# Kernel optimization log

Hardware: AMD Instinct MI355X
Metric: run time of the kernel (lower is better)

Reference implementation:

```python
import jax, jax.numpy as jnp
import numpy as np

D = 128
EMB = 1024
B, S = 4, 4096


def setup_inputs() -> dict:
    key = jax.random.key(0)
    ks = jax.random.split(key, 7)
    scale = 1.0 / np.sqrt(EMB)
    return {
        "X": jax.random.normal(ks[0], (B, S, EMB), dtype=jnp.float32),
        "lam": jnp.float32(0.8),
        "Wq": jax.random.uniform(ks[1], (EMB, 2 * D), jnp.float32, -scale, scale),
        "bq": jax.random.uniform(ks[2], (2 * D,), jnp.float32, -scale, scale),
        "Wk": jax.random.uniform(ks[3], (EMB, 2 * D), jnp.float32, -scale, scale),
        "bk": jax.random.uniform(ks[4], (2 * D,), jnp.float32, -scale, scale),
        "Wv": jax.random.uniform(ks[5], (EMB, D), jnp.float32, -scale, scale),
        "bv": jax.random.uniform(ks[6], (D,), jnp.float32, -scale, scale),
    }


def reference(X, lam, Wq, bq, Wk, bk, Wv, bv):
    # Projections: Q,K are [B,S,2d]; V is [B,S,d]
    Q = X @ Wq + bq
    K = X @ Wk + bk
    V = X @ Wv + bv
    Q1, Q2 = Q[..., :D], Q[..., D:]
    K1, K2 = K[..., :D], K[..., D:]
    s = 1.0 / jnp.sqrt(jnp.float32(D))
    # Dual QK^T scores [B,S,S]
    A1 = jnp.einsum("bqd,bkd->bqk", Q1, K1) * s
    A2 = jnp.einsum("bqd,bkd->bqk", Q2, K2) * s
    P = jax.nn.softmax(A1, axis=-1) - lam * jax.nn.softmax(A2, axis=-1)
    return jnp.einsum("bqk,bkd->bqd", P, V)
```

## Files before the change

kernel.cpp:

```cpp
#include <hip/hip_runtime.h>
#include <hip/hip_bf16.h>


typedef __attribute__((ext_vector_type(8))) short bf16x8;
typedef __attribute__((ext_vector_type(4))) float f32x4;
typedef __attribute__((ext_vector_type(16))) float f32x16;

#define MFMA16(a, b, c) __builtin_amdgcn_mfma_f32_16x16x32_bf16((a), (b), (c), 0, 0, 0)
#define MFMA32(a, b, c) __builtin_amdgcn_mfma_f32_32x32x16_bf16((a), (b), (c), 0, 0, 0)

typedef const __attribute__((address_space(1))) void gas_void;
typedef __attribute__((address_space(3))) void las_void;
#define GLOAD16(G, L) __builtin_amdgcn_global_load_lds((gas_void*)(G), (las_void*)(L), 16, 0, 0)

__device__ __forceinline__ unsigned short f2bf(float x) {
    union { float f; unsigned u; } v; v.f = x;
    return (unsigned short)((v.u + 0x7FFFu + ((v.u >> 16) & 1u)) >> 16);
}
__device__ __forceinline__ unsigned pk2bf(float a, float b) {
    __hip_bfloat162 h = __float22bfloat162_rn(float2{a, b});
    union { __hip_bfloat162 h2; unsigned u; } cv; cv.h2 = h;
    return cv.u;
}
__device__ __forceinline__ float fexp2(float x) {
    float r; asm("v_exp_f32 %0, %1" : "=v"(r) : "v"(x)); return r;
}

__global__ __launch_bounds__(256) void wtrans_kernel(
    const float* __restrict__ Wq, const float* __restrict__ Wk,
    const float* __restrict__ Wv, unsigned short* __restrict__ Wt) {
    int tid = blockIdx.x * 256 + threadIdx.x;
    int k = tid & 1023, n = tid >> 10;
    float v;
    if (n < 256)      v = Wq[k * 256 + n];
    else if (n < 512) v = Wk[k * 256 + (n - 256)];
    else              v = Wv[k * 128 + (n - 512)];
    Wt[tid] = f2bf(v);
}

__global__ __launch_bounds__(256) void proj_kernel(
    const float* __restrict__ X, const unsigned short* __restrict__ Wt,
    const float* __restrict__ bq, const float* __restrict__ bk,
    const float* __restrict__ bv,
    unsigned short* __restrict__ Qs, unsigned short* __restrict__ Kb,
    unsigned short* __restrict__ Vb) {
    __shared__ alignas(16) char lds[16384];
    const int nt = blockIdx.y;
    const int m0 = blockIdx.x * 128;
    const int t = threadIdx.x, w = t >> 6, l = t & 63, c = l & 15, g = l >> 4;
    const int wm = w >> 1, wn = w & 1;
    const unsigned short* Wrow = Wt + (long)(nt * 128) * 1024;

    f32x4 acc[4][4];
    const f32x4 fz = {0.f, 0.f, 0.f, 0.f};
#pragma unroll
    for (int i = 0; i < 4; i++)
#pragma unroll
        for (int j = 0; j < 4; j++) acc[i][j] = fz;

    const int srow = t >> 1, sh = t & 1;
    const int sswz = (srow & 7) << 4;
    for (int k0 = 0; k0 < 1024; k0 += 32) {
        const float* xs = X + (long)(m0 + srow) * 1024 + k0 + sh * 16;
        float4 f0 = *(const float4*)(xs + 0);
        float4 f1 = *(const float4*)(xs + 4);
        float4 f2 = *(const float4*)(xs + 8);
        float4 f3 = *(const float4*)(xs + 12);
        const unsigned short* wsc = Wrow + (long)srow * 1024 + k0 + sh * 16;
        uint4 w0 = *(const uint4*)(wsc + 0);
        uint4 w1 = *(const uint4*)(wsc + 8);
        uint4 xa, xb;
        xa.x = pk2bf(f0.x, f0.y); xa.y = pk2bf(f0.z, f0.w);
        xa.z = pk2bf(f1.x, f1.y); xa.w = pk2bf(f1.z, f1.w);
        xb.x = pk2bf(f2.x, f2.y); xb.y = pk2bf(f2.z, f2.w);
        xb.z = pk2bf(f3.x, f3.y); xb.w = pk2bf(f3.z, f3.w);
        int base = srow * 64 + sh * 32;
        *(uint4*)(lds + ((base + 0) ^ sswz)) = xa;
        *(uint4*)(lds + ((base + 16) ^ sswz)) = xb;
        *(uint4*)(lds + 8192 + ((base + 0) ^ sswz)) = w0;
        *(uint4*)(lds + 8192 + ((base + 16) ^ sswz)) = w1;
        __syncthreads();

        bf16x8 af[4];
#pragma unroll
        for (int am = 0; am < 4; am++) {
            int r_ = wm * 64 + am * 16 + c;
            af[am] = *(const bf16x8*)(lds + ((r_ * 64 + g * 16) ^ ((c & 7) << 4)));
        }
#pragma unroll
        for (int bn = 0; bn < 4; bn++) {
            int r_ = wn * 64 + bn * 16 + c;
            bf16x8 bfr = *(const bf16x8*)(lds + 8192 + ((r_ * 64 + g * 16) ^ ((c & 7) << 4)));
#pragma unroll
            for (int am = 0; am < 4; am++) acc[am][bn] = MFMA16(af[am], bfr, acc[am][bn]);
        }
        __syncthreads();
    }

    const float QSCALE = 0.08838834764831845f * 1.4426950408889634f;
    const float* bias; float scale; unsigned short* outp; int ostride, ocol0, boff;
    if (nt < 2)      { bias = bq; boff = nt * 128;       scale = QSCALE; outp = Qs; ostride = 256; ocol0 = nt * 128; }
    else if (nt < 4) { bias = bk; boff = (nt - 2) * 128; scale = 1.0f;   outp = Kb; ostride = 256; ocol0 = (nt - 2) * 128; }
    else             { bias = bv; boff = 0;              scale = 1.0f;   outp = Vb; ostride = 128; ocol0 = 0; }
#pragma unroll
    for (int bn = 0; bn < 4; bn++) {
        int ncol = wn * 64 + bn * 16 + c;
        float bb = bias[boff + ncol];
#pragma unroll
        for (int am = 0; am < 4; am++) {
#pragma unroll
            for (int r = 0; r < 4; r++) {
                long row = m0 + wm * 64 + am * 16 + 4 * g + r;
                outp[row * ostride + ocol0 + ncol] = f2bf((acc[am][bn][r] + bb) * scale);
            }
        }
    }
}

__global__ __launch_bounds__(256) void vtrans_kernel(
    const unsigned short* __restrict__ Vb, unsigned short* __restrict__ Vt) {
    int tid = blockIdx.x * 256 + threadIdx.x;
    int s = tid & 4095, d = (tid >> 12) & 127, b = tid >> 19;
    Vt[tid] = Vb[(((long)b << 12) + s) * 128 + d];
}

__global__ __launch_bounds__(256) void attn3_kernel(
    const unsigned short* __restrict__ Qs, const unsigned short* __restrict__ Kb,
    const unsigned short* __restrict__ Vt,
    float* __restrict__ Po, float* __restrict__ Ps, int nsplit, int ks) {
    __shared__ alignas(16) char lds[49152];
    const int t = threadIdx.x;
    const int w = t >> 6, l = t & 63, r31 = l & 31, hi = l >> 5;

    const int total = gridDim.x;
    const int lin = (blockIdx.x & 7) * (total >> 3) + (blockIdx.x >> 3);
    const int qb = lin & 31;
    const int g2 = lin >> 5;
    const int br = g2 & 1;
    const int sp = g2 >> 1;
    const int split = sp % nsplit, b = sp / nsplit;

    const long qrow = (long)b * 4096 + qb * 128 + w * 32 + r31;
    bf16x8 qf[8];
    const unsigned short* Qp = Qs + qrow * 256 + br * 128 + hi * 8;
#pragma unroll
    for (int ds = 0; ds < 8; ds++) qf[ds] = *(const bf16x8*)(Qp + ds * 16);

    f32x16 o[4];
    const f32x16 oz = {};
#pragma unroll
    for (int dt = 0; dt < 4; dt++) o[dt] = oz;
    float m = -1e30f, s = 0.f;

    const int krowA = t >> 4;
    const int kcolS = (((t & 15) * 16) - krowA * 16) & 255;
    const int vdA = t >> 2;
    const int vcolS = (((t & 3) * 16) - (((vdA >> 1) & 3) * 16)) & 63;
    const long kbb = (long)b * 4096;
    const char* kSrc0 = (const char*)Kb + (kbb + krowA) * 512 + br * 256 + kcolS;
    const char* vSrc0 = (const char*)Vt + ((long)b * 128 + vdA) * 8192 + vcolS;
    char* dst0 = lds + w * 1024;

    const int kb0 = split * ks;
    const int nt = ks >> 5;
#define STAGE(KB_, BUF_)                                                       \
    {                                                                          \
        const char* kp_ = kSrc0 + (long)(KB_)*512;                             \
        const char* vp_ = vSrc0 + (long)(KB_)*2;                               \
        char* d_ = dst0 + (BUF_)*16384;                                        \
        GLOAD16(kp_, d_);                                                      \
        GLOAD16(kp_ + 8192, d_ + 4096);                                        \
        GLOAD16(vp_, d_ + 8192);                                               \
        GLOAD16(vp_ + 524288, d_ + 12288);                                     \
    }

    int kro[8];
#pragma unroll
    for (int ds = 0; ds < 8; ds++)
        kro[ds] = r31 * 256 + ((ds * 32 + hi * 16 + r31 * 16) & 255);
    int vro0[4], vro1[4];
#pragma unroll
    for (int dt = 0; dt < 4; dt++) {
        int vr = dt * 32 + r31, rot = ((vr >> 1) & 3) * 16;
        vro0[dt] = 8192 + vr * 64 + ((hi * 16 + rot) & 63);
        vro1[dt] = 8192 + vr * 64 + ((32 + hi * 16 + rot) & 63);
    }

    STAGE(kb0, 0);
    STAGE(kb0 + 32, 1);
    int cb = 0, sb = 2;

    for (int it = 0; it < nt; it++) {
        asm volatile("s_waitcnt vmcnt(4)" ::: "memory");
        __builtin_amdgcn_sched_barrier(0);
        __builtin_amdgcn_s_barrier();
        __builtin_amdgcn_sched_barrier(0);
        {
            int i2 = it + 2;
            int kn = (i2 < nt) ? kb0 + (i2 << 5) : kb0;
            STAGE(kn, sb);
        }
        const char* bufp = lds + cb * 16384;

        f32x16 pa = oz, pb_ = oz;
        __builtin_amdgcn_s_setprio(1);
#pragma unroll
        for (int ds = 0; ds < 4; ds++) {
            bf16x8 kfa = *(const bf16x8*)(bufp + kro[ds]);
            bf16x8 kfb = *(const bf16x8*)(bufp + kro[ds + 4]);
            pa = MFMA32(kfa, qf[ds], pa);
            pb_ = MFMA32(kfb, qf[ds + 4], pb_);
        }
        __builtin_amdgcn_s_setprio(0);
        f32x16 p;
#pragma unroll
        for (int i = 0; i < 16; i++) p[i] = pa[i] + pb_[i];

        float m0_ = fmaxf(fmaxf(p[0], p[1]), p[2]);
        float m1_ = fmaxf(fmaxf(p[3], p[4]), p[5]);
        float m2_ = fmaxf(fmaxf(p[6], p[7]), p[8]);
        float m3_ = fmaxf(fmaxf(p[9], p[10]), p[11]);
        float m4_ = fmaxf(fmaxf(p[12], p[13]), p[14]);
        float lmx = fmaxf(fmaxf(fmaxf(fmaxf(m0_, m1_), m2_),
                                fmaxf(m3_, m4_)), p[15]);
        lmx = fmaxf(lmx, __shfl_xor(lmx, 32));
        if (__any(lmx > m + 8.f)) {
            float mn = fmaxf(m, lmx);
            float al = fexp2(m - mn);
            s *= al; m = mn;
#pragma unroll
            for (int dt = 0; dt < 4; dt++) o[dt] *= al;
        }
        float pe[16];
#pragma unroll
        for (int i = 0; i < 16; i++) pe[i] = fexp2(p[i] - m);
        float s0 = (pe[0] + pe[1]) + (pe[2] + pe[3]);
        float s1 = (pe[4] + pe[5]) + (pe[6] + pe[7]);
        float s2 = (pe[8] + pe[9]) + (pe[10] + pe[11]);
        float s3 = (pe[12] + pe[13]) + (pe[14] + pe[15]);
        float ps_ = (s0 + s1) + (s2 + s3);
        ps_ += __shfl_xor(ps_, 32);
        s += ps_;

        unsigned cA = pk2bf(pe[0], pe[1]), cB = pk2bf(pe[2], pe[3]);
        unsigned cC = pk2bf(pe[4], pe[5]), cD = pk2bf(pe[6], pe[7]);
        asm volatile("v_permlane32_swap_b32 %0, %1" : "+v"(cA), "+v"(cC));
        asm volatile("v_permlane32_swap_b32 %0, %1" : "+v"(cB), "+v"(cD));
        unsigned dA = pk2bf(pe[8], pe[9]), dB = pk2bf(pe[10], pe[11]);
        unsigned dC = pk2bf(pe[12], pe[13]), dD = pk2bf(pe[14], pe[15]);
        asm volatile("v_permlane32_swap_b32 %0, %1" : "+v"(dA), "+v"(dC));
        asm volatile("v_permlane32_swap_b32 %0, %1" : "+v"(dB), "+v"(dD));
        union { uint4 u; bf16x8 v; } pb0, pb1;
        pb0.u = uint4{cA, cB, cC, cD};
        pb1.u = uint4{dA, dB, dC, dD};

        __builtin_amdgcn_s_setprio(1);
#pragma unroll
        for (int dt = 0; dt < 4; dt++) {
            bf16x8 vf0 = *(const bf16x8*)(bufp + vro0[dt]);
            bf16x8 vf1 = *(const bf16x8*)(bufp + vro1[dt]);
            o[dt] = MFMA32(vf0, pb0.v, o[dt]);
            o[dt] = MFMA32(vf1, pb1.v, o[dt]);
        }
        __builtin_amdgcn_s_setprio(0);
        cb = (cb == 2) ? 0 : cb + 1;
        sb = (sb == 2) ? 0 : sb + 1;
    }
    asm volatile("s_waitcnt vmcnt(0)" ::: "memory");

    float* po = Po + ((qrow * nsplit + split) * 2 + br) * 128;
#pragma unroll
    for (int dt = 0; dt < 4; dt++) {
#pragma unroll
        for (int rg = 0; rg < 4; rg++) {
            float4 v;
            v.x = o[dt][rg * 4 + 0];
            v.y = o[dt][rg * 4 + 1];
            v.z = o[dt][rg * 4 + 2];
            v.w = o[dt][rg * 4 + 3];
            *(float4*)(po + dt * 32 + rg * 8 + hi * 4) = v;
        }
    }
    if (hi == 0)
        *(float2*)(Ps + (qrow * nsplit + split) * 4 + br * 2) = float2{m, s};
#undef STAGE
}

__global__ __launch_bounds__(256) void combine_kernel(
    const float* __restrict__ Po, const float* __restrict__ Ps,
    const float* __restrict__ lam_p, float* __restrict__ out, int nsplit) {
    int tid = blockIdx.x * 256 + threadIdx.x;
    int q = tid >> 5, dq = (tid & 31) * 4;
    float M1 = -1e30f, M2 = -1e30f;
    for (int s = 0; s < nsplit; s++) {
        float4 st = *(const float4*)(Ps + (long)(q * nsplit + s) * 4);
        M1 = fmaxf(M1, st.x); M2 = fmaxf(M2, st.z);
    }
    float S1 = 0.f, S2 = 0.f;
    float a0 = 0.f, a1 = 0.f, a2 = 0.f, a3 = 0.f;
    float b0 = 0.f, b1 = 0.f, b2 = 0.f, b3 = 0.f;
    for (int s = 0; s < nsplit; s++) {
        float4 st = *(const float4*)(Ps + (long)(q * nsplit + s) * 4);
        float w1 = fexp2(st.x - M1), w2 = fexp2(st.z - M2);
        S1 += st.y * w1; S2 += st.w * w2;
        const float* p1 = Po + (((long)q * nsplit + s) * 2 + 0) * 128 + dq;
        const float* p2 = Po + (((long)q * nsplit + s) * 2 + 1) * 128 + dq;
        float4 v1 = *(const float4*)p1;
        float4 v2 = *(const float4*)p2;
        a0 += v1.x * w1; a1 += v1.y * w1; a2 += v1.z * w1; a3 += v1.w * w1;
        b0 += v2.x * w2; b1 += v2.y * w2; b2 += v2.z * w2; b3 += v2.w * w2;
    }
    float lam = *lam_p;
    float i1 = 1.f / S1, i2 = lam / S2;
    float4 v;
    v.x = a0 * i1 - b0 * i2;
    v.y = a1 * i1 - b1 * i2;
    v.z = a2 * i1 - b2 * i2;
    v.w = a3 * i1 - b3 * i2;
    *(float4*)(out + (long)q * 128 + dq) = v;
}

extern "C" void kernel_launch(void* const* d_in, const int* in_sizes, int n_in,
                              void* d_out, int out_size, void* d_ws, size_t ws_size,
                              hipStream_t stream) {
    const float* X   = (const float*)d_in[0];
    const float* lam = (const float*)d_in[1];
    const float* Wq  = (const float*)d_in[2];
    const float* bq  = (const float*)d_in[3];
    const float* Wk  = (const float*)d_in[4];
    const float* bk  = (const float*)d_in[5];
    const float* Wv  = (const float*)d_in[6];
    const float* bv  = (const float*)d_in[7];
    char* ws = (char*)d_ws;
    unsigned short* Qs = (unsigned short*)(ws);
    unsigned short* Kb = (unsigned short*)(ws + (8u << 20));
    unsigned short* Vb = (unsigned short*)(ws + (16u << 20));
    unsigned short* Vt = (unsigned short*)(ws + (20u << 20));
    unsigned short* Wt = (unsigned short*)(ws + (24u << 20));
    const size_t base = (size_t)26 << 20;
    const size_t NQ = 16384;
    int nsplit = 1;
    if (ws_size >= base + NQ * 4 * 2 * 128 * 4 + NQ * 4 * 4 * 4)      nsplit = 4;
    else if (ws_size >= base + NQ * 2 * 2 * 128 * 4 + NQ * 2 * 4 * 4) nsplit = 2;
    float* Po = (float*)(ws + base);
    float* Ps = (float*)(ws + base + NQ * (size_t)nsplit * 2 * 128 * 4);

    wtrans_kernel<<<2560, 256, 0, stream>>>(Wq, Wk, Wv, Wt);
    proj_kernel<<<dim3(128, 5), 256, 0, stream>>>(X, Wt, bq, bk, bv, Qs, Kb, Vb);
    vtrans_kernel<<<8192, 256, 0, stream>>>(Vb, Vt);
    attn3_kernel<<<256 * nsplit, 256, 0, stream>>>(Qs, Kb, Vt, Po, Ps,
                                                   nsplit, 4096 / nsplit);
    combine_kernel<<<2048, 256, 0, stream>>>(Po, Ps, lam, (float*)d_out, nsplit);
}
```

Before: 170.8 us.

## Widen attention KV tile to 64 with double buffering; tile V transpose via LDS

The attention loop now processes 64 keys per iteration instead of 32. It uses two 32 KB LDS buffers instead of three 16 KB ones, and sets launch bounds to two blocks per CU. The aim is to halve the barrier count and the softmax bookkeeping per key and to give the MFMA units more independent work. In exchange the prefetch waits for vmcnt(0) at each iteration, so prefetch depth and overlap shrink. Separately, the V transpose becomes a tiled LDS kernel with 16-byte coalesced loads and stores, replacing the scalar strided gather.

```diff
diff --git a/kernel.cpp b/kernel.cpp
--- a/kernel.cpp
+++ b/kernel.cpp
@@ -119,16 +119,35 @@
 
 __global__ __launch_bounds__(256) void vtrans_kernel(
     const unsigned short* __restrict__ Vb, unsigned short* __restrict__ Vt) {
-    int tid = blockIdx.x * 256 + threadIdx.x;
-    int s = tid & 4095, d = (tid >> 12) & 127, b = tid >> 19;
-    Vt[tid] = Vb[(((long)b << 12) + s) * 128 + d];
-}
-
-__global__ __launch_bounds__(256) void attn3_kernel(
+    __shared__ unsigned short lds[64][72];
+    const int bid = blockIdx.x;
+    const int db = bid & 1, sb = (bid >> 1) & 63, b = bid >> 7;
+    const int s0 = sb * 64, d0 = db * 64;
+    const int t = threadIdx.x;
+    const int r = t >> 2, c4 = t & 3;
+    const unsigned short* src = Vb + ((long)(b * 4096 + s0 + r)) * 128 + d0;
+    uint4 u0 = *(const uint4*)(src + c4 * 8);
+    uint4 u1 = *(const uint4*)(src + (c4 + 4) * 8);
+    *(uint4*)(&lds[r][c4 * 8]) = u0;
+    *(uint4*)(&lds[r][(c4 + 4) * 8]) = u1;
+    __syncthreads();
+    const int dd = t >> 2;
+    unsigned short* dst = Vt + ((long)(b * 128 + d0 + dd)) * 4096 + s0;
+#pragma unroll
+    for (int cc2 = 0; cc2 < 2; cc2++) {
+        int cc = c4 + cc2 * 4;
+        unsigned short tmp[8];
+#pragma unroll
+        for (int j = 0; j < 8; j++) tmp[j] = lds[cc * 8 + j][dd];
+        *(uint4*)(dst + cc * 8) = *(const uint4*)tmp;
+    }
+}
+
+__global__ __launch_bounds__(256, 2) void attn3_kernel(
     const unsigned short* __restrict__ Qs, const unsigned short* __restrict__ Kb,
     const unsigned short* __restrict__ Vt,
     float* __restrict__ Po, float* __restrict__ Ps, int nsplit, int ks) {
-    __shared__ alignas(16) char lds[49152];
+    __shared__ alignas(16) char lds[65536];
     const int t = threadIdx.x;
     const int w = t >> 6, l = t & 63, r31 = l & 31, hi = l >> 5;
 
@@ -162,16 +181,20 @@
     char* dst0 = lds + w * 1024;
 
     const int kb0 = split * ks;
-    const int nt = ks >> 5;
+    const int nt = ks >> 6;
 #define STAGE(KB_, BUF_)                                                       \
     {                                                                          \
         const char* kp_ = kSrc0 + (long)(KB_)*512;                             \
         const char* vp_ = vSrc0 + (long)(KB_)*2;                               \
-        char* d_ = dst0 + (BUF_)*16384;                                        \
+        char* d_ = dst0 + (BUF_)*32768;                                        \
         GLOAD16(kp_, d_);                                                      \
         GLOAD16(kp_ + 8192, d_ + 4096);                                        \
-        GLOAD16(vp_, d_ + 8192);                                               \
-        GLOAD16(vp_ + 524288, d_ + 12288);                                     \
+        GLOAD16(kp_ + 16384, d_ + 8192);                                       \
+        GLOAD16(kp_ + 24576, d_ + 12288);                                      \
+        GLOAD16(vp_, d_ + 16384);                                              \
+        GLOAD16(vp_ + 524288, d_ + 20480);                                     \
+        GLOAD16(vp_ + 64, d_ + 24576);                                         \
+        GLOAD16(vp_ + 524288 + 64, d_ + 28672);                                \
     }
 
     int kro[8];
@@ -182,47 +205,48 @@
 #pragma unroll
     for (int dt = 0; dt < 4; dt++) {
         int vr = dt * 32 + r31, rot = ((vr >> 1) & 3) * 16;
-        vro0[dt] = 8192 + vr * 64 + ((hi * 16 + rot) & 63);
-        vro1[dt] = 8192 + vr * 64 + ((32 + hi * 16 + rot) & 63);
+        vro0[dt] = 16384 + vr * 64 + ((hi * 16 + rot) & 63);
+        vro1[dt] = 16384 + vr * 64 + ((32 + hi * 16 + rot) & 63);
     }
 
     STAGE(kb0, 0);
-    STAGE(kb0 + 32, 1);
-    int cb = 0, sb = 2;
 
     for (int it = 0; it < nt; it++) {
-        asm volatile("s_waitcnt vmcnt(4)" ::: "memory");
+        asm volatile("s_waitcnt vmcnt(0)" ::: "memory");
         __builtin_amdgcn_sched_barrier(0);
         __builtin_amdgcn_s_barrier();
         __builtin_amdgcn_sched_barrier(0);
-        {
-            int i2 = it + 2;
-            int kn = (i2 < nt) ? kb0 + (i2 << 5) : kb0;
-            STAGE(kn, sb);
-        }
-        const char* bufp = lds + cb * 16384;
-
-        f32x16 pa = oz, pb_ = oz;
+        if (it + 1 < nt) STAGE(kb0 + ((it + 1) << 6), (it + 1) & 1);
+        const char* bufp = lds + (it & 1) * 32768;
+
+        f32x16 pa0 = oz, pb0_ = oz, pa1 = oz, pb1_ = oz;
         __builtin_amdgcn_s_setprio(1);
 #pragma unroll
         for (int ds = 0; ds < 4; ds++) {
-            bf16x8 kfa = *(const bf16x8*)(bufp + kro[ds]);
-            bf16x8 kfb = *(const bf16x8*)(bufp + kro[ds + 4]);
-            pa = MFMA32(kfa, qf[ds], pa);
-            pb_ = MFMA32(kfb, qf[ds + 4], pb_);
+            bf16x8 k0a = *(const bf16x8*)(bufp + kro[ds]);
+            bf16x8 k0b = *(const bf16x8*)(bufp + kro[ds + 4]);
+            bf16x8 k1a = *(const bf16x8*)(bufp + 8192 + kro[ds]);
+            bf16x8 k1b = *(const bf16x8*)(bufp + 8192 + kro[ds + 4]);
+            pa0 = MFMA32(k0a, qf[ds], pa0);
+            pb0_ = MFMA32(k0b, qf[ds + 4], pb0_);
+            pa1 = MFMA32(k1a, qf[ds], pa1);
+            pb1_ = MFMA32(k1b, qf[ds + 4], pb1_);
         }
         __builtin_amdgcn_s_setprio(0);
-        f32x16 p;
-#pragma unroll
-        for (int i = 0; i < 16; i++) p[i] = pa[i] + pb_[i];
-
-        float m0_ = fmaxf(fmaxf(p[0], p[1]), p[2]);
-        float m1_ = fmaxf(fmaxf(p[3], p[4]), p[5]);
-        float m2_ = fmaxf(fmaxf(p[6], p[7]), p[8]);
-        float m3_ = fmaxf(fmaxf(p[9], p[10]), p[11]);
-        float m4_ = fmaxf(fmaxf(p[12], p[13]), p[14]);
-        float lmx = fmaxf(fmaxf(fmaxf(fmaxf(m0_, m1_), m2_),
-                                fmaxf(m3_, m4_)), p[15]);
+        f32x16 p0, p1;
+#pragma unroll
+        for (int i = 0; i < 16; i++) { p0[i] = pa0[i] + pb0_[i]; p1[i] = pa1[i] + pb1_[i]; }
+
+        float x0 = fmaxf(fmaxf(p0[0], p0[1]), fmaxf(p0[2], p0[3]));
+        float x1 = fmaxf(fmaxf(p0[4], p0[5]), fmaxf(p0[6], p0[7]));
+        float x2 = fmaxf(fmaxf(p0[8], p0[9]), fmaxf(p0[10], p0[11]));
+        float x3 = fmaxf(fmaxf(p0[12], p0[13]), fmaxf(p0[14], p0[15]));
+        float y0 = fmaxf(fmaxf(p1[0], p1[1]), fmaxf(p1[2], p1[3]));
+        float y1 = fmaxf(fmaxf(p1[4], p1[5]), fmaxf(p1[6], p1[7]));
+        float y2 = fmaxf(fmaxf(p1[8], p1[9]), fmaxf(p1[10], p1[11]));
+        float y3 = fmaxf(fmaxf(p1[12], p1[13]), fmaxf(p1[14], p1[15]));
+        float lmx = fmaxf(fmaxf(fmaxf(x0, x1), fmaxf(x2, x3)),
+                          fmaxf(fmaxf(y0, y1), fmaxf(y2, y3)));
         lmx = fmaxf(lmx, __shfl_xor(lmx, 32));
         if (__any(lmx > m + 8.f)) {
             float mn = fmaxf(m, lmx);
@@ -231,42 +255,57 @@
 #pragma unroll
             for (int dt = 0; dt < 4; dt++) o[dt] *= al;
         }
-        float pe[16];
-#pragma unroll
-        for (int i = 0; i < 16; i++) pe[i] = fexp2(p[i] - m);
-        float s0 = (pe[0] + pe[1]) + (pe[2] + pe[3]);
-        float s1 = (pe[4] + pe[5]) + (pe[6] + pe[7]);
-        float s2 = (pe[8] + pe[9]) + (pe[10] + pe[11]);
-        float s3 = (pe[12] + pe[13]) + (pe[14] + pe[15]);
+        float pe0[16], pe1[16];
+#pragma unroll
+        for (int i = 0; i < 16; i++) { pe0[i] = fexp2(p0[i] - m); pe1[i] = fexp2(p1[i] - m); }
+        float s0 = ((pe0[0] + pe0[1]) + (pe0[2] + pe0[3])) +
+                   ((pe0[4] + pe0[5]) + (pe0[6] + pe0[7]));
+        float s1 = ((pe0[8] + pe0[9]) + (pe0[10] + pe0[11])) +
+                   ((pe0[12] + pe0[13]) + (pe0[14] + pe0[15]));
+        float s2 = ((pe1[0] + pe1[1]) + (pe1[2] + pe1[3])) +
+                   ((pe1[4] + pe1[5]) + (pe1[6] + pe1[7]));
+        float s3 = ((pe1[8] + pe1[9]) + (pe1[10] + pe1[11])) +
+                   ((pe1[12] + pe1[13]) + (pe1[14] + pe1[15]));
         float ps_ = (s0 + s1) + (s2 + s3);
         ps_ += __shfl_xor(ps_, 32);
         s += ps_;
 
-        unsigned cA = pk2bf(pe[0], pe[1]), cB = pk2bf(pe[2], pe[3]);
-        unsigned cC = pk2bf(pe[4], pe[5]), cD = pk2bf(pe[6], pe[7]);
+        unsigned cA = pk2bf(pe0[0], pe0[1]), cB = pk2bf(pe0[2], pe0[3]);
+        unsigned cC = pk2bf(pe0[4], pe0[5]), cD = pk2bf(pe0[6], pe0[7]);
         asm volatile("v_permlane32_swap_b32 %0, %1" : "+v"(cA), "+v"(cC));
         asm volatile("v_permlane32_swap_b32 %0, %1" : "+v"(cB), "+v"(cD));
-        unsigned dA = pk2bf(pe[8], pe[9]), dB = pk2bf(pe[10], pe[11]);
-        unsigned dC = pk2bf(pe[12], pe[13]), dD = pk2bf(pe[14], pe[15]);
+        unsigned dA = pk2bf(pe0[8], pe0[9]), dB = pk2bf(pe0[10], pe0[11]);
+        unsigned dC = pk2bf(pe0[12], pe0[13]), dD = pk2bf(pe0[14], pe0[15]);
         asm volatile("v_permlane32_swap_b32 %0, %1" : "+v"(dA), "+v"(dC));
         asm volatile("v_permlane32_swap_b32 %0, %1" : "+v"(dB), "+v"(dD));
-        union { uint4 u; bf16x8 v; } pb0, pb1;
-        pb0.u = uint4{cA, cB, cC, cD};
-        pb1.u = uint4{dA, dB, dC, dD};
+        unsigned eA = pk2bf(pe1[0], pe1[1]), eB = pk2bf(pe1[2], pe1[3]);
+        unsigned eC = pk2bf(pe1[4], pe1[5]), eD = pk2bf(pe1[6], pe1[7]);
+        asm volatile("v_permlane32_swap_b32 %0, %1" : "+v"(eA), "+v"(eC));
+        asm volatile("v_permlane32_swap_b32 %0, %1" : "+v"(eB), "+v"(eD));
+        unsigned fA = pk2bf(pe1[8], pe1[9]), fB = pk2bf(pe1[10], pe1[11]);
+        unsigned fC = pk2bf(pe1[12], pe1[13]), fD = pk2bf(pe1[14], pe1[15]);
+        asm volatile("v_permlane32_swap_b32 %0, %1" : "+v"(fA), "+v"(fC));
+        asm volatile("v_permlane32_swap_b32 %0, %1" : "+v"(fB), "+v"(fD));
+        union { uint4 u; bf16x8 v; } q00, q01, q10, q11;
+        q00.u = uint4{cA, cB, cC, cD};
+        q01.u = uint4{dA, dB, dC, dD};
+        q10.u = uint4{eA, eB, eC, eD};
+        q11.u = uint4{fA, fB, fC, fD};
 
         __builtin_amdgcn_s_setprio(1);
 #pragma unroll
         for (int dt = 0; dt < 4; dt++) {
-            bf16x8 vf0 = *(const bf16x8*)(bufp + vro0[dt]);
-            bf16x8 vf1 = *(const bf16x8*)(bufp + vro1[dt]);
-            o[dt] = MFMA32(vf0, pb0.v, o[dt]);
-            o[dt] = MFMA32(vf1, pb1.v, o[dt]);
+            bf16x8 v00 = *(const bf16x8*)(bufp + vro0[dt]);
+            bf16x8 v01 = *(const bf16x8*)(bufp + vro1[dt]);
+            bf16x8 v10 = *(const bf16x8*)(bufp + 8192 + vro0[dt]);
+            bf16x8 v11 = *(const bf16x8*)(bufp + 8192 + vro1[dt]);
+            o[dt] = MFMA32(v00, q00.v, o[dt]);
+            o[dt] = MFMA32(v01, q01.v, o[dt]);
+            o[dt] = MFMA32(v10, q10.v, o[dt]);
+            o[dt] = MFMA32(v11, q11.v, o[dt]);
         }
         __builtin_amdgcn_s_setprio(0);
-        cb = (cb == 2) ? 0 : cb + 1;
-        sb = (sb == 2) ? 0 : sb + 1;
-    }
-    asm volatile("s_waitcnt vmcnt(0)" ::: "memory");
+    }
 
     float* po = Po + ((qrow * nsplit + split) * 2 + br) * 128;
 #pragma unroll
@@ -347,7 +386,7 @@
 
     wtrans_kernel<<<2560, 256, 0, stream>>>(Wq, Wk, Wv, Wt);
     proj_kernel<<<dim3(128, 5), 256, 0, stream>>>(X, Wt, bq, bk, bv, Qs, Kb, Vb);
-    vtrans_kernel<<<8192, 256, 0, stream>>>(Vb, Vt);
+    vtrans_kernel<<<512, 256, 0, stream>>>(Vb, Vt);
     attn3_kernel<<<256 * nsplit, 256, 0, stream>>>(Qs, Kb, Vt, Po, Ps,
                                                    nsplit, 4096 / nsplit);
     combine_kernel<<<2048, 256, 0, stream>>>(Po, Ps, lam, (float*)d_out, nsplit);
```

Measured after the change: 157.4 us, median of 2. 1.09x faster.

## Split key tiles across wave pairs in attention and tile V transpose through LDS

Applied to the files above, without the earlier changes.

The attention kernel goes from 256 to 512 threads per block. Each pair of waves shares one 32-row query group and handles alternating 32-key tiles, with four LDS buffers loaded two tiles at a time. At the end the partial softmax states of each pair are merged through LDS. The V transpose becomes a tiled LDS transpose with vectorized loads and stores instead of a strided scalar gather. The goal is more waves in flight to hide latency. The costs are larger LDS use, a full vmcnt(0) wait each iteration, and an extra reduction step.

```diff
diff --git a/kernel.cpp b/kernel.cpp
--- a/kernel.cpp
+++ b/kernel.cpp
@@ -119,18 +119,38 @@
 
 __global__ __launch_bounds__(256) void vtrans_kernel(
     const unsigned short* __restrict__ Vb, unsigned short* __restrict__ Vt) {
-    int tid = blockIdx.x * 256 + threadIdx.x;
-    int s = tid & 4095, d = (tid >> 12) & 127, b = tid >> 19;
-    Vt[tid] = Vb[(((long)b << 12) + s) * 128 + d];
-}
-
-__global__ __launch_bounds__(256) void attn3_kernel(
+    __shared__ unsigned short lds[64][72];
+    const int bid = blockIdx.x;
+    const int db = bid & 1, sb = (bid >> 1) & 63, b = bid >> 7;
+    const int s0 = sb * 64, d0 = db * 64;
+    const int t = threadIdx.x;
+    const int r = t >> 2, c4 = t & 3;
+    const unsigned short* src = Vb + ((long)(b * 4096 + s0 + r)) * 128 + d0;
+    uint4 u0 = *(const uint4*)(src + c4 * 8);
+    uint4 u1 = *(const uint4*)(src + (c4 + 4) * 8);
+    *(uint4*)(&lds[r][c4 * 8]) = u0;
+    *(uint4*)(&lds[r][(c4 + 4) * 8]) = u1;
+    __syncthreads();
+    const int dd = t >> 2;
+    unsigned short* dst = Vt + ((long)(b * 128 + d0 + dd)) * 4096 + s0;
+#pragma unroll
+    for (int cc2 = 0; cc2 < 2; cc2++) {
+        int cc = c4 + cc2 * 4;
+        unsigned short tmp[8];
+#pragma unroll
+        for (int j = 0; j < 8; j++) tmp[j] = lds[cc * 8 + j][dd];
+        *(uint4*)(dst + cc * 8) = *(const uint4*)tmp;
+    }
+}
+
+__global__ __launch_bounds__(512, 4) void attn5_kernel(
     const unsigned short* __restrict__ Qs, const unsigned short* __restrict__ Kb,
     const unsigned short* __restrict__ Vt,
     float* __restrict__ Po, float* __restrict__ Ps, int nsplit, int ks) {
-    __shared__ alignas(16) char lds[49152];
+    __shared__ alignas(16) char lds[67584];
     const int t = threadIdx.x;
     const int w = t >> 6, l = t & 63, r31 = l & 31, hi = l >> 5;
+    const int wq = w >> 1, kh = w & 1;
 
     const int total = gridDim.x;
     const int lin = (blockIdx.x & 7) * (total >> 3) + (blockIdx.x >> 3);
@@ -140,7 +160,7 @@
     const int sp = g2 >> 1;
     const int split = sp % nsplit, b = sp / nsplit;
 
-    const long qrow = (long)b * 4096 + qb * 128 + w * 32 + r31;
+    const long qrow = (long)b * 4096 + qb * 128 + wq * 32 + r31;
     bf16x8 qf[8];
     const unsigned short* Qp = Qs + qrow * 256 + br * 128 + hi * 8;
 #pragma unroll
@@ -152,26 +172,25 @@
     for (int dt = 0; dt < 4; dt++) o[dt] = oz;
     float m = -1e30f, s = 0.f;
 
-    const int krowA = t >> 4;
-    const int kcolS = (((t & 15) * 16) - krowA * 16) & 255;
-    const int vdA = t >> 2;
-    const int vcolS = (((t & 3) * 16) - (((vdA >> 1) & 3) * 16)) & 63;
+    const int krow = t >> 4;
+    const int ksrc_rot = (((t & 15) * 16) - krow * 16) & 255;
+    const int vd = t >> 2;
+    const int vcolS = (((t & 3) * 16) - (((vd >> 1) & 3) * 16)) & 63;
     const long kbb = (long)b * 4096;
-    const char* kSrc0 = (const char*)Kb + (kbb + krowA) * 512 + br * 256 + kcolS;
-    const char* vSrc0 = (const char*)Vt + ((long)b * 128 + vdA) * 8192 + vcolS;
+    const char* kSrc0 = (const char*)Kb + (kbb + krow) * 512 + br * 256 + ksrc_rot;
+    const char* vSrc0 = (const char*)Vt + ((long)b * 128 + vd) * 8192 + vcolS;
     char* dst0 = lds + w * 1024;
 
     const int kb0 = split * ks;
     const int nt = ks >> 5;
+    const int nj = nt >> 1;
 #define STAGE(KB_, BUF_)                                                       \
     {                                                                          \
         const char* kp_ = kSrc0 + (long)(KB_)*512;                             \
         const char* vp_ = vSrc0 + (long)(KB_)*2;                               \
         char* d_ = dst0 + (BUF_)*16384;                                        \
         GLOAD16(kp_, d_);                                                      \
-        GLOAD16(kp_ + 8192, d_ + 4096);                                        \
         GLOAD16(vp_, d_ + 8192);                                               \
-        GLOAD16(vp_ + 524288, d_ + 12288);                                     \
     }
 
     int kro[8];
@@ -188,19 +207,19 @@
 
     STAGE(kb0, 0);
     STAGE(kb0 + 32, 1);
-    int cb = 0, sb = 2;
-
-    for (int it = 0; it < nt; it++) {
-        asm volatile("s_waitcnt vmcnt(4)" ::: "memory");
+
+    for (int j = 0; j < nj; j++) {
+        asm volatile("s_waitcnt vmcnt(0)" ::: "memory");
         __builtin_amdgcn_sched_barrier(0);
         __builtin_amdgcn_s_barrier();
         __builtin_amdgcn_sched_barrier(0);
-        {
-            int i2 = it + 2;
-            int kn = (i2 < nt) ? kb0 + (i2 << 5) : kb0;
-            STAGE(kn, sb);
-        }
-        const char* bufp = lds + cb * 16384;
+        if (j + 1 < nj) {
+            int base = kb0 + ((j + 1) << 6);
+            STAGE(base, (2 * j + 2) & 3);
+            STAGE(base + 32, (2 * j + 3) & 3);
+        }
+        const int ti = 2 * j + kh;
+        const char* bufp = lds + (ti & 3) * 16384;
 
         f32x16 pa = oz, pb_ = oz;
         __builtin_amdgcn_s_setprio(1);
@@ -216,13 +235,11 @@
 #pragma unroll
         for (int i = 0; i < 16; i++) p[i] = pa[i] + pb_[i];
 
-        float m0_ = fmaxf(fmaxf(p[0], p[1]), p[2]);
-        float m1_ = fmaxf(fmaxf(p[3], p[4]), p[5]);
-        float m2_ = fmaxf(fmaxf(p[6], p[7]), p[8]);
-        float m3_ = fmaxf(fmaxf(p[9], p[10]), p[11]);
-        float m4_ = fmaxf(fmaxf(p[12], p[13]), p[14]);
-        float lmx = fmaxf(fmaxf(fmaxf(fmaxf(m0_, m1_), m2_),
-                                fmaxf(m3_, m4_)), p[15]);
+        float x0 = fmaxf(fmaxf(p[0], p[1]), fmaxf(p[2], p[3]));
+        float x1 = fmaxf(fmaxf(p[4], p[5]), fmaxf(p[6], p[7]));
+        float x2 = fmaxf(fmaxf(p[8], p[9]), fmaxf(p[10], p[11]));
+        float x3 = fmaxf(fmaxf(p[12], p[13]), fmaxf(p[14], p[15]));
+        float lmx = fmaxf(fmaxf(x0, x1), fmaxf(x2, x3));
         lmx = fmaxf(lmx, __shfl_xor(lmx, 32));
         if (__any(lmx > m + 8.f)) {
             float mn = fmaxf(m, lmx);
@@ -263,26 +280,60 @@
             o[dt] = MFMA32(vf1, pb1.v, o[dt]);
         }
         __builtin_amdgcn_s_setprio(0);
-        cb = (cb == 2) ? 0 : cb + 1;
-        sb = (sb == 2) ? 0 : sb + 1;
-    }
-    asm volatile("s_waitcnt vmcnt(0)" ::: "memory");
-
-    float* po = Po + ((qrow * nsplit + split) * 2 + br) * 128;
-#pragma unroll
-    for (int dt = 0; dt < 4; dt++) {
-#pragma unroll
-        for (int rg = 0; rg < 4; rg++) {
-            float4 v;
-            v.x = o[dt][rg * 4 + 0];
-            v.y = o[dt][rg * 4 + 1];
-            v.z = o[dt][rg * 4 + 2];
-            v.w = o[dt][rg * 4 + 3];
-            *(float4*)(po + dt * 32 + rg * 8 + hi * 4) = v;
-        }
-    }
-    if (hi == 0)
-        *(float2*)(Ps + (qrow * nsplit + split) * 4 + br * 2) = float2{m, s};
+    }
+
+    __syncthreads();
+    if (kh == 1) {
+        char* obase = lds + wq * 16384 + l * 256;
+#pragma unroll
+        for (int dt = 0; dt < 4; dt++) {
+#pragma unroll
+            for (int rg = 0; rg < 4; rg++) {
+                f32x4 v;
+                v[0] = o[dt][rg * 4 + 0];
+                v[1] = o[dt][rg * 4 + 1];
+                v[2] = o[dt][rg * 4 + 2];
+                v[3] = o[dt][rg * 4 + 3];
+                *(f32x4*)(obase + (((dt * 4 + rg) * 16 + l * 16) & 255)) = v;
+            }
+        }
+        *(float2*)(lds + 65536 + (wq * 64 + l) * 8) = float2{m, s};
+    }
+    __syncthreads();
+    if (kh == 0) {
+        float2 ms1 = *(const float2*)(lds + 65536 + (wq * 64 + l) * 8);
+        float mstar = fmaxf(m, ms1.x);
+        float a0 = fexp2(m - mstar), a1 = fexp2(ms1.x - mstar);
+        s = s * a0 + ms1.y * a1;
+        m = mstar;
+        const char* obase = lds + wq * 16384 + l * 256;
+#pragma unroll
+        for (int dt = 0; dt < 4; dt++) {
+#pragma unroll
+            for (int rg = 0; rg < 4; rg++) {
+                f32x4 v1 = *(const f32x4*)(obase + (((dt * 4 + rg) * 16 + l * 16) & 255));
+                o[dt][rg * 4 + 0] = o[dt][rg * 4 + 0] * a0 + v1[0] * a1;
+                o[dt][rg * 4 + 1] = o[dt][rg * 4 + 1] * a0 + v1[1] * a1;
+                o[dt][rg * 4 + 2] = o[dt][rg * 4 + 2] * a0 + v1[2] * a1;
+                o[dt][rg * 4 + 3] = o[dt][rg * 4 + 3] * a0 + v1[3] * a1;
+            }
+        }
+        float* po = Po + ((qrow * nsplit + split) * 2 + br) * 128;
+#pragma unroll
+        for (int dt = 0; dt < 4; dt++) {
+#pragma unroll
+            for (int rg = 0; rg < 4; rg++) {
+                float4 v;
+                v.x = o[dt][rg * 4 + 0];
+                v.y = o[dt][rg * 4 + 1];
+                v.z = o[dt][rg * 4 + 2];
+                v.w = o[dt][rg * 4 + 3];
+                *(float4*)(po + dt * 32 + rg * 8 + hi * 4) = v;
+            }
+        }
+        if (hi == 0)
+            *(float2*)(Ps + (qrow * nsplit + split) * 4 + br * 2) = float2{m, s};
+    }
 #undef STAGE
 }
 
@@ -347,8 +398,8 @@
 
     wtrans_kernel<<<2560, 256, 0, stream>>>(Wq, Wk, Wv, Wt);
     proj_kernel<<<dim3(128, 5), 256, 0, stream>>>(X, Wt, bq, bk, bv, Qs, Kb, Vb);
-    vtrans_kernel<<<8192, 256, 0, stream>>>(Vb, Vt);
-    attn3_kernel<<<256 * nsplit, 256, 0, stream>>>(Qs, Kb, Vt, Po, Ps,
+    vtrans_kernel<<<512, 256, 0, stream>>>(Vb, Vt);
+    attn5_kernel<<<256 * nsplit, 512, 0, stream>>>(Qs, Kb, Vt, Po, Ps,
                                                    nsplit, 4096 / nsplit);
     combine_kernel<<<2048, 256, 0, stream>>>(Po, Ps, lam, (float*)d_out, nsplit);
 }
```

Result: slower. 256.1 us (+49.9%).
